# Kernel tuning notes

Measured on AMD Instinct MI355X. Metric: run time of the kernel, lower is better.

The kernel has to match this reference:

```python
import jax, jax.numpy as jnp
import numpy as np

B, N, F, K = 16384, 64, 128, 64


def setup_inputs() -> dict:
    key = jax.random.key(0)
    kx, kd = jax.random.split(key)
    x = jax.random.normal(kx, (B, F), dtype=jnp.float32)
    D = jax.random.normal(kd, (N, F, K), dtype=jnp.float32)  # per-cluster factor dictionaries
    return {"x": x, "D": D}


def reference(x, D):
    # --- assignment step (torch.no_grad in original) ---
    # Dtx[n,b,j] = sum_i D[n,i,j] * x[b,i]
    Dtx = jnp.einsum('nij,bi->nbj', D, x)                      # [N,B,K]
    # per-cluster (D^T D)^{-1}, batched inverse over the cluster axis
    DTD = jnp.einsum('nij,nik->njk', D, D)                     # [N,K,K]
    DTD_inv = jnp.linalg.inv(DTD)                              # [N,K,K]
    Cs = jnp.einsum('nbj,nkj->nbk', Dtx, DTD_inv)              # [N,B,K]
    x_hat = jnp.einsum('nij,nbj->nbi', D, Cs)                  # [N,B,F]
    # nearest-subspace assignment per sample
    label = jnp.argmin(jnp.linalg.norm(x_hat - x[None], axis=-1), axis=0)  # [B] int
    C = Cs[label, jnp.arange(x.shape[0])]                      # [B,K] gather per sample
    # --- reconstruction loss: sum_i || x[i] - D[label[i]] @ C[i] ||^2 ---
    x_rec = jnp.einsum('bik,bk->bi', D[label], C)              # grouped gather + matmul
    se_loss = jnp.sum(jnp.square(x - x_rec))
    return se_loss, label
```

## Files before the change

### kernel.cpp

```cpp
#include <hip/hip_runtime.h>
#include <hip/hip_bf16.h>

#define B_N 16384
#define TAU 0.25f
#define GS 68
#define YS 133

typedef float f32x4 __attribute__((ext_vector_type(4)));
typedef short s16x8 __attribute__((ext_vector_type(8)));

__device__ __forceinline__ void gl_lds16(const void* g, void* l) {
    __builtin_amdgcn_global_load_lds(
        (const __attribute__((address_space(1))) void*)g,
        (__attribute__((address_space(3))) void*)l, 16, 0, 0);
}

__device__ __forceinline__ unsigned short bf16_bits(float v) {
    __hip_bfloat16 h = __float2bfloat16(v);
    return *reinterpret_cast<unsigned short*>(&h);
}

__global__ __launch_bounds__(256) void prep_convert(const float* __restrict__ x,
                                                    const float* __restrict__ D,
                                                    unsigned short* __restrict__ xh,
                                                    float* __restrict__ nrm,
                                                    float* __restrict__ Qg,
                                                    unsigned short* __restrict__ Bht,
                                                    float* __restrict__ out) {
    const int t = threadIdx.x;

    if (blockIdx.x >= 64) {
        const int gid = (blockIdx.x - 64) * 256 + t;
        if (gid == 0) out[0] = 0.0f;
        const size_t base = (size_t)gid * 32;
        float s = 0.0f;
        #pragma unroll
        for (int c = 0; c < 8; ++c) {
            const f32x4 v = ((const f32x4*)(x + base))[c];
            s += v.x * v.x + v.y * v.y + v.z * v.z + v.w * v.w;
            ushort4 h;
            h.x = bf16_bits(v.x); h.y = bf16_bits(v.y);
            h.z = bf16_bits(v.z); h.w = bf16_bits(v.w);
            ((ushort4*)(xh + base))[c] = h;
        }
        s += __shfl_xor(s, 1, 64);
        s += __shfl_xor(s, 2, 64);
        if ((gid & 3) == 0) nrm[gid >> 2] = s;
        return;
    }

    __shared__ float Y[64 * YS];
    __shared__ __align__(16) float G[64 * GS + 64];
    __shared__ __align__(16) float Lti[8 * 8 * 8];
    const int n = blockIdx.x;
    const float* Dn = D + (size_t)n * 8192;

    for (int e4 = t; e4 < 2048; e4 += 256) {
        const int c = e4 >> 4, j4 = (e4 & 15) * 4;
        const f32x4 v = ((const f32x4*)Dn)[e4];
        Y[(j4 + 0) * YS + c] = v.x;
        Y[(j4 + 1) * YS + c] = v.y;
        Y[(j4 + 2) * YS + c] = v.z;
        Y[(j4 + 3) * YS + c] = v.w;
    }

    {
        const int a0 = (t & 15) * 4, b0 = (t >> 4) * 4;
        float acc[4][4] = {};
        #pragma unroll 4
        for (int i = 0; i < 128; ++i) {
            const f32x4 av = *(const f32x4*)(Dn + i * 64 + a0);
            const f32x4 bv = *(const f32x4*)(Dn + i * 64 + b0);
            const float aa[4] = {av.x, av.y, av.z, av.w};
            const float bb[4] = {bv.x, bv.y, bv.z, bv.w};
            #pragma unroll
            for (int p = 0; p < 4; ++p)
                #pragma unroll
                for (int q = 0; q < 4; ++q) acc[p][q] = fmaf(aa[p], bb[q], acc[p][q]);
        }
        #pragma unroll
        for (int p = 0; p < 4; ++p)
            #pragma unroll
            for (int q = 0; q < 4; ++q) G[(a0 + p) * GS + b0 + q] = acc[p][q];
    }
    __syncthreads();

    for (int p8 = 0; p8 < 8; ++p8) {
        const int pb = p8 * 8;
        if (t < 64) {
            const int lane = t;
            const f32x4 v0 = *(const f32x4*)&G[lane * GS + pb];
            const f32x4 v1 = *(const f32x4*)&G[lane * GS + pb + 4];
            float g[8] = {v0.x, v0.y, v0.z, v0.w, v1.x, v1.y, v1.z, v1.w};
            #pragma unroll
            for (int kk = 0; kk < 8; ++kk) {
                const int k = pb + kk;
                const float dk = __shfl(g[kk], k, 64);
                const float rinv = 1.0f / sqrtf(dk);
                const float lik = g[kk] * rinv;
                g[kk] = lik;
                if (lane == 0) G[64 * GS + k] = rinv;
                #pragma unroll
                for (int jj = kk + 1; jj < 8; ++jj) {
                    const float ljk = __shfl(lik, pb + jj, 64);
                    g[jj] -= lik * ljk;
                }
            }
            *(f32x4*)&G[lane * GS + pb]     = (f32x4){g[0], g[1], g[2], g[3]};
            *(f32x4*)&G[lane * GS + pb + 4] = (f32x4){g[4], g[5], g[6], g[7]};
        }
        __syncthreads();
        const int base = pb + 8;
        if (base < 64) {
            for (int i = base + (t >> 5); i < 64; i += 8) {
                const f32x4 Li0 = *(const f32x4*)&G[i * GS + pb];
                const f32x4 Li1 = *(const f32x4*)&G[i * GS + pb + 4];
                for (int j = base + (t & 31); j < 64; j += 32) {
                    const f32x4 Lj0 = *(const f32x4*)&G[j * GS + pb];
                    const f32x4 Lj1 = *(const f32x4*)&G[j * GS + pb + 4];
                    float s = G[i * GS + j];
                    s -= Li0.x * Lj0.x + Li0.y * Lj0.y + Li0.z * Lj0.z + Li0.w * Lj0.w;
                    s -= Li1.x * Lj1.x + Li1.y * Lj1.y + Li1.z * Lj1.z + Li1.w * Lj1.w;
                    G[i * GS + j] = s;
                }
            }
        }
        __syncthreads();
    }

    if (t < 64) {
        const int bi = t >> 3, c = t & 7;
        const int base = bi * 8;
        float m[8];
        #pragma unroll
        for (int r = 0; r < 8; ++r) {
            float s = (r == c) ? 1.0f : 0.0f;
            #pragma unroll
            for (int k = 0; k < r; ++k)
                s -= G[(base + r) * GS + base + k] * m[k];
            m[r] = s * G[64 * GS + base + r];
        }
        #pragma unroll
        for (int r = 0; r < 8; ++r) Lti[(base + r) * 8 + c] = m[r];
    }
    __syncthreads();

    if (t < 128) {
        const int c = t;
        for (int i = 0; i < 8; ++i) {
            float Tv[8];
            #pragma unroll
            for (int r = 0; r < 8; ++r) Tv[r] = Y[(i * 8 + r) * YS + c];
            for (int k = 0; k < i; ++k) {
                #pragma unroll
                for (int kk = 0; kk < 8; ++kk) {
                    const float z = Y[(k * 8 + kk) * YS + c];
                    #pragma unroll
                    for (int r = 0; r < 8; ++r)
                        Tv[r] -= G[(i * 8 + r) * GS + k * 8 + kk] * z;
                }
            }
            #pragma unroll
            for (int r = 0; r < 8; ++r) {
                float z = 0.0f;
                #pragma unroll
                for (int rp = 0; rp <= r; ++rp)
                    z += Lti[(i * 8 + r) * 8 + rp] * Tv[rp];
                Y[(i * 8 + r) * YS + c] = z;
            }
        }
    }
    __syncthreads();

    for (int e = t; e < 8192; e += 256) {
        const int j = e >> 7, i = e & 127;
        Bht[((size_t)n * 64 + j) * 128 + i] = bf16_bits(Y[j * YS + i]);
    }
    for (int e = t; e < 8192; e += 256) {
        const int i = e >> 6, j = e & 63;
        Qg[(size_t)n * 8192 + e] = Y[j * YS + i];
    }
}

__global__ __launch_bounds__(256) void gemm_scores(const unsigned short* __restrict__ xh,
                                                   const unsigned short* __restrict__ Bht,
                                                   float* __restrict__ S) {
    __shared__ unsigned short ldsA[128 * 128];
    __shared__ unsigned short ldsB[64 * 128];
    const int t = threadIdx.x, w = t >> 6, lane = t & 63;
    const int m0 = blockIdx.x * 128;
    const int n0 = blockIdx.y * 8;
    const int lm = lane & 15, lg = lane >> 4;

    {
        const int rl = lane >> 4, p = lane & 15;
        #pragma unroll
        for (int q = 0; q < 8; ++q) {
            const int row = w * 32 + q * 4 + rl;
            const int c = p ^ (row & 15);
            gl_lds16(xh + (size_t)(m0 + row) * 128 + c * 8,
                     &ldsA[(w * 32 + q * 4) * 128]);
        }
        #pragma unroll
        for (int q = 0; q < 4; ++q) {
            const int row = w * 16 + q * 4 + rl;
            const int c = p ^ (row & 15);
            gl_lds16(Bht + ((size_t)n0 * 64 + row) * 128 + c * 8,
                     &ldsB[(w * 16 + q * 4) * 128]);
        }
    }
    __syncthreads();

    s16x8 af[2][4];
    #pragma unroll
    for (int mt = 0; mt < 2; ++mt) {
        const int r = w * 32 + mt * 16 + lm;
        #pragma unroll
        for (int ks = 0; ks < 4; ++ks) {
            const int p = (ks * 4 + lg) ^ (r & 15);
            af[mt][ks] = *(const s16x8*)&ldsA[r * 128 + p * 8];
        }
    }

    #pragma unroll 1
    for (int it = 0; it < 8; ++it) {
        const int nc = n0 + it;

        s16x8 bf[4][4];
        #pragma unroll
        for (int nt = 0; nt < 4; ++nt) {
            const int r = nt * 16 + lm;
            #pragma unroll
            for (int ks = 0; ks < 4; ++ks) {
                const int p = (ks * 4 + lg) ^ (r & 15);
                bf[nt][ks] = *(const s16x8*)&ldsB[r * 128 + p * 8];
            }
        }
        __syncthreads();

        if (it < 7) {
            const int rl = lane >> 4, p = lane & 15;
            #pragma unroll
            for (int q = 0; q < 4; ++q) {
                const int row = w * 16 + q * 4 + rl;
                const int c = p ^ (row & 15);
                gl_lds16(Bht + ((size_t)(nc + 1) * 64 + row) * 128 + c * 8,
                         &ldsB[(w * 16 + q * 4) * 128]);
            }
        }

        #pragma unroll
        for (int mt = 0; mt < 2; ++mt) {
            f32x4 acc[4];
            #pragma unroll
            for (int nt = 0; nt < 4; ++nt) acc[nt] = (f32x4){0.f, 0.f, 0.f, 0.f};
            #pragma unroll
            for (int ks = 0; ks < 4; ++ks)
                #pragma unroll
                for (int nt = 0; nt < 4; ++nt)
                    acc[nt] = __builtin_amdgcn_mfma_f32_16x16x32_bf16(
                        af[mt][ks], bf[nt][ks], acc[nt], 0, 0, 0);
            #pragma unroll
            for (int rg = 0; rg < 4; ++rg) {
                float p = 0.0f;
                #pragma unroll
                for (int nt = 0; nt < 4; ++nt) {
                    const float v = acc[nt][rg];
                    p += v * v;
                }
                p += __shfl_xor(p, 1, 64);
                p += __shfl_xor(p, 2, 64);
                p += __shfl_xor(p, 4, 64);
                p += __shfl_xor(p, 8, 64);
                if (lm == 0)
                    S[(size_t)nc * B_N + m0 + w * 32 + mt * 16 + lg * 4 + rg] = p;
            }
        }
        __syncthreads();
    }
}

__global__ __launch_bounds__(256) void argmax_rescore(const float* __restrict__ Sa,
                                                      const float* __restrict__ nrm,
                                                      const float* __restrict__ x,
                                                      const float* __restrict__ Qg,
                                                      float* __restrict__ out) {
    __shared__ float tile[32 * 65];
    __shared__ int sflags[32];
    __shared__ int scnt;
    __shared__ float ssum;
    __shared__ float scorr[4];
    const int t = threadIdx.x, w = t >> 6, lane = t & 63;
    const int b0 = blockIdx.x * 32;
    if (t == 0) scnt = 0;

    for (int e = t; e < 512; e += 256) {
        const int n = e >> 3, c4 = e & 7;
        const f32x4 v = *(const f32x4*)&Sa[(size_t)n * B_N + b0 + c4 * 4];
        tile[(c4 * 4 + 0) * 65 + n] = v.x;
        tile[(c4 * 4 + 1) * 65 + n] = v.y;
        tile[(c4 * 4 + 2) * 65 + n] = v.z;
        tile[(c4 * 4 + 3) * 65 + n] = v.w;
    }
    __syncthreads();

    if (t < 32) {
        float v1 = -1e30f, v2 = -1e30f;
        int n1 = 0;
        for (int n = 0; n < 64; ++n) {
            const float v = tile[t * 65 + n];
            if (v > v1) { v2 = v1; v1 = v; n1 = n; }
            else v2 = fmaxf(v2, v);
        }
        out[1 + b0 + t] = (float)n1;
        if (v1 - v2 < TAU) { const int i = atomicAdd(&scnt, 1); sflags[i] = t; }
        float err = nrm[b0 + t] - v1;
        err += __shfl_xor(err, 1, 64);
        err += __shfl_xor(err, 2, 64);
        err += __shfl_xor(err, 4, 64);
        err += __shfl_xor(err, 8, 64);
        err += __shfl_xor(err, 16, 64);
        if (t == 0) ssum = err;
    }
    if (lane == 0) scorr[w] = 0.0f;
    __syncthreads();

    const int nf = scnt;
    float corr = 0.0f;
    for (int f = w; f < nf; f += 4) {
        const int s = sflags[f];
        const int b2 = b0 + s;
        const float v = tile[s * 65 + lane];
        float vm = v;
        for (int off = 32; off; off >>= 1) vm = fmaxf(vm, __shfl_xor(vm, off, 64));
        unsigned long long mask = __ballot((vm - v) < TAU);
        float best = -1e30f;
        int bn = 0;
        while (mask) {
            const int nn = (int)__builtin_ctzll(mask);
            mask &= mask - 1;
            const float* Qn = Qg + (size_t)nn * 8192;
            const float* xb = x + (size_t)b2 * 128;
            float d0 = 0.0f, d1 = 0.0f, d2 = 0.0f, d3 = 0.0f;
            #pragma unroll
            for (int i = 0; i < 128; i += 4) {
                d0 = fmaf(Qn[(i + 0) * 64 + lane], xb[i + 0], d0);
                d1 = fmaf(Qn[(i + 1) * 64 + lane], xb[i + 1], d1);
                d2 = fmaf(Qn[(i + 2) * 64 + lane], xb[i + 2], d2);
                d3 = fmaf(Qn[(i + 3) * 64 + lane], xb[i + 3], d3);
            }
            const float dot = (d0 + d1) + (d2 + d3);
            float sv = dot * dot;
            for (int off = 32; off; off >>= 1) sv += __shfl_xor(sv, off, 64);
            if (sv > best) { best = sv; bn = nn; }
        }
        if (lane == 0) {
            out[1 + b2] = (float)bn;
            corr += vm - best;
        }
    }
    if (lane == 0 && corr != 0.0f) scorr[w] += corr;
    __syncthreads();
    if (t == 0)
        atomicAdd(out, ssum + scorr[0] + scorr[1] + scorr[2] + scorr[3]);
}

extern "C" void kernel_launch(void* const* d_in, const int* in_sizes, int n_in,
                              void* d_out, int out_size, void* d_ws, size_t ws_size,
                              hipStream_t stream) {
    const float* x = (const float*)d_in[0];
    const float* D = (const float*)d_in[1];
    float* out = (float*)d_out;

    char* ws = (char*)d_ws;
    unsigned short* xh  = (unsigned short*)(ws);
    unsigned short* Bht = (unsigned short*)(ws + (4u << 20));
    float* Qg           = (float*)(ws + (5u << 20));
    float* Sa           = (float*)(ws + (7u << 20));
    float* nrm          = (float*)(ws + (11u << 20));

    prep_convert<<<320, 256, 0, stream>>>(x, D, xh, nrm, Qg, Bht, out);
    gemm_scores<<<dim3(128, 8), 256, 0, stream>>>(xh, Bht, Sa);
    argmax_rescore<<<512, 256, 0, stream>>>(Sa, nrm, x, Qg, out);
}
```

Baseline: 158.3 us.

## Widen prep kernel to 512 threads and replace triangular solve with explicit inverse GEMM

The prep kernel now runs with 512 threads per block. The Gram matrix accumulation is split into two halves over the feature dimension and then summed, and the blocked triangular solve (previously 128 threads looping serially over blocks) is replaced. In its place, the full inverse of the Cholesky factor is built in parallel inside the upper triangle of G, and a 4x4-tiled product of that inverse with D^T produces the Qg and Bht outputs with vectorized stores. The goal is to spread the serial, latency-bound per-cluster setup across more threads. The cost is extra barriers, more arithmetic, and possible register pressure under the 512-thread launch bound.

```diff
diff --git a/kernel.cpp b/kernel.cpp
--- a/kernel.cpp
+++ b/kernel.cpp
@@ -4,7 +4,7 @@
 #define B_N 16384
 #define TAU 0.25f
 #define GS 68
-#define YS 133
+#define YS 132
 
 typedef float f32x4 __attribute__((ext_vector_type(4)));
 typedef short s16x8 __attribute__((ext_vector_type(8)));
@@ -20,7 +20,7 @@
     return *reinterpret_cast<unsigned short*>(&h);
 }
 
-__global__ __launch_bounds__(256) void prep_convert(const float* __restrict__ x,
+__global__ __launch_bounds__(512) void prep_convert(const float* __restrict__ x,
                                                     const float* __restrict__ D,
                                                     unsigned short* __restrict__ xh,
                                                     float* __restrict__ nrm,
@@ -30,7 +30,7 @@
     const int t = threadIdx.x;
 
     if (blockIdx.x >= 64) {
-        const int gid = (blockIdx.x - 64) * 256 + t;
+        const int gid = (blockIdx.x - 64) * 512 + t;
         if (gid == 0) out[0] = 0.0f;
         const size_t base = (size_t)gid * 32;
         float s = 0.0f;
@@ -55,7 +55,7 @@
     const int n = blockIdx.x;
     const float* Dn = D + (size_t)n * 8192;
 
-    for (int e4 = t; e4 < 2048; e4 += 256) {
+    for (int e4 = t; e4 < 2048; e4 += 512) {
         const int c = e4 >> 4, j4 = (e4 & 15) * 4;
         const f32x4 v = ((const f32x4*)Dn)[e4];
         Y[(j4 + 0) * YS + c] = v.x;
@@ -65,10 +65,12 @@
     }
 
     {
-        const int a0 = (t & 15) * 4, b0 = (t >> 4) * 4;
+        const int h = t >> 8;
+        const int a0 = (t & 15) * 4, b0 = ((t >> 4) & 15) * 4;
+        const int i0 = h * 64;
         float acc[4][4] = {};
         #pragma unroll 4
-        for (int i = 0; i < 128; ++i) {
+        for (int i = i0; i < i0 + 64; ++i) {
             const f32x4 av = *(const f32x4*)(Dn + i * 64 + a0);
             const f32x4 bv = *(const f32x4*)(Dn + i * 64 + b0);
             const float aa[4] = {av.x, av.y, av.z, av.w};
@@ -78,10 +80,19 @@
                 #pragma unroll
                 for (int q = 0; q < 4; ++q) acc[p][q] = fmaf(aa[p], bb[q], acc[p][q]);
         }
-        #pragma unroll
-        for (int p = 0; p < 4; ++p)
-            #pragma unroll
-            for (int q = 0; q < 4; ++q) G[(a0 + p) * GS + b0 + q] = acc[p][q];
+        if (h == 0) {
+            #pragma unroll
+            for (int p = 0; p < 4; ++p)
+                #pragma unroll
+                for (int q = 0; q < 4; ++q) G[(a0 + p) * GS + b0 + q] = acc[p][q];
+        }
+        __syncthreads();
+        if (h == 1) {
+            #pragma unroll
+            for (int p = 0; p < 4; ++p)
+                #pragma unroll
+                for (int q = 0; q < 4; ++q) G[(a0 + p) * GS + b0 + q] += acc[p][q];
+        }
     }
     __syncthreads();
 
@@ -112,7 +123,7 @@
         __syncthreads();
         const int base = pb + 8;
         if (base < 64) {
-            for (int i = base + (t >> 5); i < 64; i += 8) {
+            for (int i = base + (t >> 5); i < 64; i += 16) {
                 const f32x4 Li0 = *(const f32x4*)&G[i * GS + pb];
                 const f32x4 Li1 = *(const f32x4*)&G[i * GS + pb + 4];
                 for (int j = base + (t & 31); j < 64; j += 32) {
@@ -145,40 +156,74 @@
     }
     __syncthreads();
 
-    if (t < 128) {
-        const int c = t;
-        for (int i = 0; i < 8; ++i) {
-            float Tv[8];
-            #pragma unroll
-            for (int r = 0; r < 8; ++r) Tv[r] = Y[(i * 8 + r) * YS + c];
-            for (int k = 0; k < i; ++k) {
-                #pragma unroll
-                for (int kk = 0; kk < 8; ++kk) {
-                    const float z = Y[(k * 8 + kk) * YS + c];
+    {
+        const int j = t >> 3, r = t & 7, jb = j >> 3;
+        const float rinvj = G[64 * GS + j];
+        for (int m8 = 0; m8 < 8; ++m8) {
+            if (m8 >= jb) {
+                const int g = m8 * 8 + r;
+                float wv = (g == j) ? 1.0f : 0.0f;
+                for (int mm = jb; mm < m8; ++mm) {
                     #pragma unroll
-                    for (int r = 0; r < 8; ++r)
-                        Tv[r] -= G[(i * 8 + r) * GS + k * 8 + kk] * z;
+                    for (int kk = 0; kk < 8; ++kk) {
+                        const int gp = mm * 8 + kk;
+                        const float liv = (gp > j) ? G[j * GS + gp]
+                                         : ((gp == j) ? rinvj : 0.0f);
+                        wv -= G[g * GS + gp] * liv;
+                    }
                 }
-            }
-            #pragma unroll
-            for (int r = 0; r < 8; ++r) {
                 float z = 0.0f;
                 #pragma unroll
-                for (int rp = 0; rp <= r; ++rp)
-                    z += Lti[(i * 8 + r) * 8 + rp] * Tv[rp];
-                Y[(i * 8 + r) * YS + c] = z;
-            }
-        }
-    }
-    __syncthreads();
-
-    for (int e = t; e < 8192; e += 256) {
-        const int j = e >> 7, i = e & 127;
-        Bht[((size_t)n * 64 + j) * 128 + i] = bf16_bits(Y[j * YS + i]);
-    }
-    for (int e = t; e < 8192; e += 256) {
-        const int i = e >> 6, j = e & 63;
-        Qg[(size_t)n * 8192 + e] = Y[j * YS + i];
+                for (int rp = 0; rp < 8; ++rp) {
+                    const float wrp = __shfl(wv, (t & 56) | rp, 64);
+                    z = fmaf(Lti[g * 8 + rp], wrp, z);
+                }
+                if (g > j) G[j * GS + g] = z;
+            }
+            __syncthreads();
+        }
+    }
+
+    {
+        const int j0 = (t >> 5) * 4, c0 = (t & 31) * 4;
+        const f32x4 rv4 = *(const f32x4*)&G[64 * GS + j0];
+        float acc[4][4] = {};
+        #pragma unroll 4
+        for (int k = 0; k < j0; ++k) {
+            const f32x4 lv = *(const f32x4*)&G[k * GS + j0];
+            const f32x4 yv = *(const f32x4*)&Y[k * YS + c0];
+            #pragma unroll
+            for (int ej = 0; ej < 4; ++ej)
+                #pragma unroll
+                for (int ec = 0; ec < 4; ++ec)
+                    acc[ej][ec] = fmaf(lv[ej], yv[ec], acc[ej][ec]);
+        }
+        #pragma unroll
+        for (int kt = 0; kt < 4; ++kt) {
+            const int k = j0 + kt;
+            const f32x4 lq = *(const f32x4*)&G[k * GS + j0];
+            const f32x4 yv = *(const f32x4*)&Y[k * YS + c0];
+            #pragma unroll
+            for (int ej = 0; ej < 4; ++ej) {
+                const int jj = j0 + ej;
+                const float lsel = (jj > k) ? lq[ej] : ((jj == k) ? rv4[ej] : 0.0f);
+                #pragma unroll
+                for (int ec = 0; ec < 4; ++ec)
+                    acc[ej][ec] = fmaf(lsel, yv[ec], acc[ej][ec]);
+            }
+        }
+        #pragma unroll
+        for (int ec = 0; ec < 4; ++ec) {
+            *(f32x4*)&Qg[(size_t)n * 8192 + (c0 + ec) * 64 + j0] =
+                (f32x4){acc[0][ec], acc[1][ec], acc[2][ec], acc[3][ec]};
+        }
+        #pragma unroll
+        for (int ej = 0; ej < 4; ++ej) {
+            ushort4 h;
+            h.x = bf16_bits(acc[ej][0]); h.y = bf16_bits(acc[ej][1]);
+            h.z = bf16_bits(acc[ej][2]); h.w = bf16_bits(acc[ej][3]);
+            *(ushort4*)&Bht[((size_t)n * 64 + j0 + ej) * 128 + c0] = h;
+        }
     }
 }
 
@@ -379,7 +424,7 @@
     float* Sa           = (float*)(ws + (7u << 20));
     float* nrm          = (float*)(ws + (11u << 20));
 
-    prep_convert<<<320, 256, 0, stream>>>(x, D, xh, nrm, Qg, Bht, out);
+    prep_convert<<<192, 512, 0, stream>>>(x, D, xh, nrm, Qg, Bht, out);
     gemm_scores<<<dim3(128, 8), 256, 0, stream>>>(xh, Bht, Sa);
     argmax_rescore<<<512, 256, 0, stream>>>(Sa, nrm, x, Qg, out);
 }
```

New measurement: 156.4 us. About the same (-1.2%).

## Fuse score GEMM with argmax and rescore, keeping cluster scores in LDS

Applied to the files above, without the earlier changes.

Merges the score GEMM and the argmax/rescore kernels into one kernel. Each block takes 64 samples, and its four waves each cover 16 clusters. Cluster projection fragments are loaded straight from global memory into registers with double buffering, while the sample fragments stay resident. Scores go to LDS instead of a 4 MB global buffer, and per-wave top-2 results are merged in shared memory. This removes one launch and the global round trip of the score matrix. The cost is higher register pressure and repeated global loads of Bht in every block.

```diff
diff --git a/kernel.cpp b/kernel.cpp
--- a/kernel.cpp
+++ b/kernel.cpp
@@ -182,155 +182,148 @@
     }
 }
 
-__global__ __launch_bounds__(256) void gemm_scores(const unsigned short* __restrict__ xh,
+__global__ __launch_bounds__(256) void gemm_argmax(const unsigned short* __restrict__ xh,
                                                    const unsigned short* __restrict__ Bht,
-                                                   float* __restrict__ S) {
-    __shared__ unsigned short ldsA[128 * 128];
-    __shared__ unsigned short ldsB[64 * 128];
-    const int t = threadIdx.x, w = t >> 6, lane = t & 63;
-    const int m0 = blockIdx.x * 128;
-    const int n0 = blockIdx.y * 8;
-    const int lm = lane & 15, lg = lane >> 4;
-
-    {
-        const int rl = lane >> 4, p = lane & 15;
-        #pragma unroll
-        for (int q = 0; q < 8; ++q) {
-            const int row = w * 32 + q * 4 + rl;
-            const int c = p ^ (row & 15);
-            gl_lds16(xh + (size_t)(m0 + row) * 128 + c * 8,
-                     &ldsA[(w * 32 + q * 4) * 128]);
-        }
-        #pragma unroll
-        for (int q = 0; q < 4; ++q) {
-            const int row = w * 16 + q * 4 + rl;
-            const int c = p ^ (row & 15);
-            gl_lds16(Bht + ((size_t)n0 * 64 + row) * 128 + c * 8,
-                     &ldsB[(w * 16 + q * 4) * 128]);
-        }
-    }
-    __syncthreads();
-
-    s16x8 af[2][4];
-    #pragma unroll
-    for (int mt = 0; mt < 2; ++mt) {
-        const int r = w * 32 + mt * 16 + lm;
-        #pragma unroll
-        for (int ks = 0; ks < 4; ++ks) {
-            const int p = (ks * 4 + lg) ^ (r & 15);
-            af[mt][ks] = *(const s16x8*)&ldsA[r * 128 + p * 8];
-        }
-    }
-
-    #pragma unroll 1
-    for (int it = 0; it < 8; ++it) {
-        const int nc = n0 + it;
-
-        s16x8 bf[4][4];
-        #pragma unroll
-        for (int nt = 0; nt < 4; ++nt) {
-            const int r = nt * 16 + lm;
-            #pragma unroll
-            for (int ks = 0; ks < 4; ++ks) {
-                const int p = (ks * 4 + lg) ^ (r & 15);
-                bf[nt][ks] = *(const s16x8*)&ldsB[r * 128 + p * 8];
-            }
-        }
-        __syncthreads();
-
-        if (it < 7) {
-            const int rl = lane >> 4, p = lane & 15;
-            #pragma unroll
-            for (int q = 0; q < 4; ++q) {
-                const int row = w * 16 + q * 4 + rl;
-                const int c = p ^ (row & 15);
-                gl_lds16(Bht + ((size_t)(nc + 1) * 64 + row) * 128 + c * 8,
-                         &ldsB[(w * 16 + q * 4) * 128]);
-            }
-        }
-
-        #pragma unroll
-        for (int mt = 0; mt < 2; ++mt) {
-            f32x4 acc[4];
-            #pragma unroll
-            for (int nt = 0; nt < 4; ++nt) acc[nt] = (f32x4){0.f, 0.f, 0.f, 0.f};
-            #pragma unroll
-            for (int ks = 0; ks < 4; ++ks)
-                #pragma unroll
-                for (int nt = 0; nt < 4; ++nt)
-                    acc[nt] = __builtin_amdgcn_mfma_f32_16x16x32_bf16(
-                        af[mt][ks], bf[nt][ks], acc[nt], 0, 0, 0);
-            #pragma unroll
-            for (int rg = 0; rg < 4; ++rg) {
-                float p = 0.0f;
-                #pragma unroll
-                for (int nt = 0; nt < 4; ++nt) {
-                    const float v = acc[nt][rg];
-                    p += v * v;
-                }
-                p += __shfl_xor(p, 1, 64);
-                p += __shfl_xor(p, 2, 64);
-                p += __shfl_xor(p, 4, 64);
-                p += __shfl_xor(p, 8, 64);
-                if (lm == 0)
-                    S[(size_t)nc * B_N + m0 + w * 32 + mt * 16 + lg * 4 + rg] = p;
-            }
-        }
-        __syncthreads();
-    }
-}
-
-__global__ __launch_bounds__(256) void argmax_rescore(const float* __restrict__ Sa,
-                                                      const float* __restrict__ nrm,
-                                                      const float* __restrict__ x,
-                                                      const float* __restrict__ Qg,
-                                                      float* __restrict__ out) {
-    __shared__ float tile[32 * 65];
-    __shared__ int sflags[32];
+                                                   const float* __restrict__ nrm,
+                                                   const float* __restrict__ x,
+                                                   const float* __restrict__ Qg,
+                                                   float* __restrict__ out) {
+    __shared__ __align__(16) unsigned short ldsA[64 * 128];
+    __shared__ float scL[64 * 65];
+    __shared__ float mrg[4][64][3];
+    __shared__ int sflags[64];
     __shared__ int scnt;
     __shared__ float ssum;
     __shared__ float scorr[4];
+
     const int t = threadIdx.x, w = t >> 6, lane = t & 63;
-    const int b0 = blockIdx.x * 32;
+    const int m0 = blockIdx.x * 64;
+    const int lm = lane & 15, lg = lane >> 4;
     if (t == 0) scnt = 0;
-
-    for (int e = t; e < 512; e += 256) {
-        const int n = e >> 3, c4 = e & 7;
-        const f32x4 v = *(const f32x4*)&Sa[(size_t)n * B_N + b0 + c4 * 4];
-        tile[(c4 * 4 + 0) * 65 + n] = v.x;
-        tile[(c4 * 4 + 1) * 65 + n] = v.y;
-        tile[(c4 * 4 + 2) * 65 + n] = v.z;
-        tile[(c4 * 4 + 3) * 65 + n] = v.w;
-    }
-    __syncthreads();
-
-    if (t < 32) {
-        float v1 = -1e30f, v2 = -1e30f;
-        int n1 = 0;
-        for (int n = 0; n < 64; ++n) {
-            const float v = tile[t * 65 + n];
-            if (v > v1) { v2 = v1; v1 = v; n1 = n; }
-            else v2 = fmaxf(v2, v);
-        }
-        out[1 + b0 + t] = (float)n1;
-        if (v1 - v2 < TAU) { const int i = atomicAdd(&scnt, 1); sflags[i] = t; }
-        float err = nrm[b0 + t] - v1;
+    if (t < 4) scorr[t] = 0.0f;
+
+    {
+        const int rl = lane >> 4, sp = lane & 15;
+        #pragma unroll
+        for (int q = 0; q < 4; ++q) {
+            const int row = w * 16 + q * 4 + rl;
+            const int c = sp ^ (row & 15);
+            gl_lds16(xh + (size_t)(m0 + row) * 128 + c * 8,
+                     &ldsA[(w * 16 + q * 4) * 128]);
+        }
+    }
+    __syncthreads();
+
+    s16x8 bfr[4][4];
+    #pragma unroll
+    for (int st = 0; st < 4; ++st) {
+        const int r = st * 16 + lm;
+        #pragma unroll
+        for (int ks = 0; ks < 4; ++ks) {
+            const int p = (ks * 4 + lg) ^ (r & 15);
+            bfr[st][ks] = *(const s16x8*)&ldsA[r * 128 + p * 8];
+        }
+    }
+
+    float v1[4] = {-1e30f, -1e30f, -1e30f, -1e30f};
+    float v2[4] = {-1e30f, -1e30f, -1e30f, -1e30f};
+    int   n1[4] = {0, 0, 0, 0};
+
+    const unsigned short* afbase = Bht + (size_t)lm * 128 + lg * 8;
+
+#define LOAD_AF(dst, cc) do {                                                   \
+    const unsigned short* bp = afbase + (size_t)(cc) * 8192;                    \
+    _Pragma("unroll")                                                           \
+    for (int mt_ = 0; mt_ < 4; ++mt_)                                           \
+        _Pragma("unroll")                                                       \
+        for (int ks_ = 0; ks_ < 4; ++ks_)                                       \
+            dst[mt_][ks_] = *(const s16x8*)(bp + mt_ * 2048 + ks_ * 32);        \
+} while (0)
+
+#define PROC(af, cc) do {                                                       \
+    _Pragma("unroll")                                                           \
+    for (int st_ = 0; st_ < 4; ++st_) {                                         \
+        f32x4 ac0 = {0.f,0.f,0.f,0.f}, ac1 = {0.f,0.f,0.f,0.f};                 \
+        f32x4 ac2 = {0.f,0.f,0.f,0.f}, ac3 = {0.f,0.f,0.f,0.f};                 \
+        _Pragma("unroll")                                                       \
+        for (int ks_ = 0; ks_ < 4; ++ks_) {                                     \
+            ac0 = __builtin_amdgcn_mfma_f32_16x16x32_bf16(af[0][ks_], bfr[st_][ks_], ac0, 0, 0, 0); \
+            ac1 = __builtin_amdgcn_mfma_f32_16x16x32_bf16(af[1][ks_], bfr[st_][ks_], ac1, 0, 0, 0); \
+            ac2 = __builtin_amdgcn_mfma_f32_16x16x32_bf16(af[2][ks_], bfr[st_][ks_], ac2, 0, 0, 0); \
+            ac3 = __builtin_amdgcn_mfma_f32_16x16x32_bf16(af[3][ks_], bfr[st_][ks_], ac3, 0, 0, 0); \
+        }                                                                       \
+        float q0 = ac0[0]*ac0[0]; q0 = fmaf(ac0[1],ac0[1],q0);                  \
+        q0 = fmaf(ac0[2],ac0[2],q0); q0 = fmaf(ac0[3],ac0[3],q0);               \
+        float q1 = ac1[0]*ac1[0]; q1 = fmaf(ac1[1],ac1[1],q1);                  \
+        q1 = fmaf(ac1[2],ac1[2],q1); q1 = fmaf(ac1[3],ac1[3],q1);               \
+        float q2 = ac2[0]*ac2[0]; q2 = fmaf(ac2[1],ac2[1],q2);                  \
+        q2 = fmaf(ac2[2],ac2[2],q2); q2 = fmaf(ac2[3],ac2[3],q2);               \
+        float q3 = ac3[0]*ac3[0]; q3 = fmaf(ac3[1],ac3[1],q3);                  \
+        q3 = fmaf(ac3[2],ac3[2],q3); q3 = fmaf(ac3[3],ac3[3],q3);               \
+        float s_ = ((q0 + q1) + q2) + q3;                                       \
+        s_ += __shfl_xor(s_, 16, 64);                                           \
+        s_ += __shfl_xor(s_, 32, 64);                                           \
+        if (lg == 0) scL[(st_ * 16 + lm) * 65 + (cc)] = s_;                     \
+        if (s_ > v1[st_]) { v2[st_] = v1[st_]; v1[st_] = s_; n1[st_] = (cc); }  \
+        else v2[st_] = fmaxf(v2[st_], s_);                                      \
+    }                                                                           \
+} while (0)
+
+    {
+        const int cb = w * 16;
+        s16x8 afA[4][4], afB[4][4];
+        LOAD_AF(afA, cb);
+        #pragma unroll 1
+        for (int ci = 0; ci < 16; ci += 2) {
+            LOAD_AF(afB, cb + ci + 1);
+            PROC(afA, cb + ci);
+            if (ci < 14) LOAD_AF(afA, cb + ci + 2);
+            PROC(afB, cb + ci + 1);
+        }
+    }
+#undef LOAD_AF
+#undef PROC
+
+    if (lg == 0) {
+        #pragma unroll
+        for (int st = 0; st < 4; ++st) {
+            mrg[w][st * 16 + lm][0] = v1[st];
+            mrg[w][st * 16 + lm][1] = v2[st];
+            mrg[w][st * 16 + lm][2] = (float)n1[st];
+        }
+    }
+    __syncthreads();
+
+    if (t < 64) {
+        float b1 = -1e30f, b2 = -1e30f;
+        int bn = 0;
+        #pragma unroll
+        for (int ww = 0; ww < 4; ++ww) {
+            const float a1 = mrg[ww][t][0];
+            const float a2 = mrg[ww][t][1];
+            const int an = (int)mrg[ww][t][2];
+            if (a1 > b1) { b2 = fmaxf(b1, a2); b1 = a1; bn = an; }
+            else b2 = fmaxf(b2, a1);
+        }
+        out[1 + m0 + t] = (float)bn;
+        if (b1 - b2 < TAU) { const int i = atomicAdd(&scnt, 1); sflags[i] = t; }
+        float err = nrm[m0 + t] - b1;
         err += __shfl_xor(err, 1, 64);
         err += __shfl_xor(err, 2, 64);
         err += __shfl_xor(err, 4, 64);
         err += __shfl_xor(err, 8, 64);
         err += __shfl_xor(err, 16, 64);
+        err += __shfl_xor(err, 32, 64);
         if (t == 0) ssum = err;
     }
-    if (lane == 0) scorr[w] = 0.0f;
     __syncthreads();
 
     const int nf = scnt;
     float corr = 0.0f;
     for (int f = w; f < nf; f += 4) {
         const int s = sflags[f];
-        const int b2 = b0 + s;
-        const float v = tile[s * 65 + lane];
+        const int b2 = m0 + s;
+        const float v = scL[s * 65 + lane];
         float vm = v;
         for (int off = 32; off; off >>= 1) vm = fmaxf(vm, __shfl_xor(vm, off, 64));
         unsigned long long mask = __ballot((vm - v) < TAU);
@@ -376,10 +369,8 @@
     unsigned short* xh  = (unsigned short*)(ws);
     unsigned short* Bht = (unsigned short*)(ws + (4u << 20));
     float* Qg           = (float*)(ws + (5u << 20));
-    float* Sa           = (float*)(ws + (7u << 20));
     float* nrm          = (float*)(ws + (11u << 20));
 
     prep_convert<<<320, 256, 0, stream>>>(x, D, xh, nrm, Qg, Bht, out);
-    gemm_scores<<<dim3(128, 8), 256, 0, stream>>>(xh, Bht, Sa);
-    argmax_rescore<<<512, 256, 0, stream>>>(Sa, nrm, x, Qg, out);
-}
+    gemm_argmax<<<256, 256, 0, stream>>>(xh, Bht, nrm, x, Qg, out);
+}
```

Measured after the change: 149.3 us. 5.7% less time.
